# Kernel tuning notes

Measured on AMD Instinct MI355X. Metric: run time of the kernel, lower is better.

Reference implementation:

```python
import jax, jax.numpy as jnp
import numpy as np

FG_THRESH = 0.5
BG_THRESH_HI = 0.5
BG_THRESH_LO = 0.1

NUM_ROIS = 8192
NUM_CLASSES = 20


def setup_inputs() -> dict:
    key = jax.random.key(0)
    k1, k2, k3, k4 = jax.random.split(key, 4)
    S = jax.random.uniform(k1, (NUM_ROIS, NUM_CLASSES), dtype=jnp.float32)
    # symmetric IoU-like matrix in [0,1] with unit diagonal
    R = jax.random.uniform(k2, (NUM_ROIS, NUM_ROIS), dtype=jnp.float32)
    U = 0.5 * (R + R.T)
    U = U.at[jnp.arange(NUM_ROIS), jnp.arange(NUM_ROIS)].set(1.0)
    # image-level multi-hot labels (float 0/1), ensure at least plausible positives
    L = (jax.random.uniform(k3, (1, NUM_CLASSES), dtype=jnp.float32) > 0.5).astype(jnp.float32)
    L = L.at[0, 0].set(1.0)  # guarantee at least one present class
    CW = jax.random.uniform(k4, (1, NUM_CLASSES), dtype=jnp.float32)
    return {"S": S, "U": U, "L": L, "CW": CW}


def reference(S, U, L, CW):
    """OICR-style ROI labeling (top_k=1 seed per present class).

    For each image-level class c with L[c] > 0, the highest-scoring ROI is the
    seed. Every ROI is assigned to the seed class with which it has maximal
    IoU. ROIs with best IoU >= fg_threshold become foreground (label c+1),
    ROIs with best IoU in [bg_thresh_lo, bg_thresh_hi) become background
    (label 0); all others are ignored (label -1, weight 0). Weights come
    from the per-class weight CW of the matched seed class.
    Returns (RL [N] int32, RW [N] float32).
    """
    valid = L[0] > 0                                   # [C]
    # seed ROI per class: argmax score (top_k = 1)
    seed_idx = jnp.argmax(S, axis=0)                   # [C]
    # IoU of every ROI to each class seed; invalid classes masked out
    iou = U[:, seed_idx]                               # [N, C]
    iou = jnp.where(valid[None, :], iou, -1.0)
    best_c = jnp.argmax(iou, axis=1)                   # [N]
    best_iou = jnp.max(iou, axis=1)                    # [N]

    is_fg = best_iou >= FG_THRESH
    is_bg = (best_iou < BG_THRESH_HI) & (best_iou >= BG_THRESH_LO)

    RL = jnp.where(is_fg, best_c.astype(jnp.int32) + 1,
                   jnp.where(is_bg, 0, -1)).astype(jnp.int32)
    w = CW[0][best_c]                                  # [N]
    RW = jnp.where(is_fg | is_bg, w, 0.0).astype(jnp.float32)
    return (RL, RW)
```

## Files before the change

kernel.cpp:

```cpp
#include <hip/hip_runtime.h>

#define NUM_ROIS 8192
#define NUM_CLASSES 20
#define FG_THRESH 0.5f
#define BG_HI 0.5f
#define BG_LO 0.1f

__global__ void roilabel_seed_argmax(const float* __restrict__ S,
                                     int* __restrict__ seeds) {
    const int c = blockIdx.x;
    const int t = threadIdx.x;

    float best_v = -__builtin_inff();
    int best_i = NUM_ROIS;

    for (int r = t; r < NUM_ROIS; r += 256) {
        float v = S[r * NUM_CLASSES + c];
        if (v > best_v) { best_v = v; best_i = r; }
    }

    __shared__ float sv[256];
    __shared__ int   si[256];
    sv[t] = best_v;
    si[t] = best_i;
    __syncthreads();

    for (int off = 128; off > 0; off >>= 1) {
        if (t < off) {
            float v2 = sv[t + off];
            int   i2 = si[t + off];
            if (v2 > sv[t] || (v2 == sv[t] && i2 < si[t])) {
                sv[t] = v2;
                si[t] = i2;
            }
        }
        __syncthreads();
    }
    if (t == 0) seeds[c] = si[0];
}

__global__ void roilabel_assign(const float* __restrict__ U,
                                const float* __restrict__ L,
                                const float* __restrict__ CW,
                                const int* __restrict__ seeds,
                                float* __restrict__ out) {
    __shared__ int   s_seed[NUM_CLASSES];
    __shared__ int   s_valid[NUM_CLASSES];
    __shared__ float s_cw[NUM_CLASSES];

    const int t = threadIdx.x;
    if (t < NUM_CLASSES) {
        s_seed[t]  = seeds[t];
        s_valid[t] = (L[t] > 0.0f) ? 1 : 0;
        s_cw[t]    = CW[t];
    }
    __syncthreads();

    const int i = blockIdx.x * blockDim.x + t;
    if (i >= NUM_ROIS) return;

    const float* __restrict__ row = U + (size_t)i * NUM_ROIS;

    float best_iou = -2.0f;
    int best_c = 0;
    #pragma unroll
    for (int c = 0; c < NUM_CLASSES; ++c) {
        float v = s_valid[c] ? row[s_seed[c]] : -1.0f;
        if (v > best_iou) { best_iou = v; best_c = c; }
    }

    const bool is_fg = (best_iou >= FG_THRESH);
    const bool is_bg = (best_iou < BG_HI) && (best_iou >= BG_LO);

    int   rl = is_fg ? (best_c + 1) : (is_bg ? 0 : -1);
    float rw = (is_fg || is_bg) ? s_cw[best_c] : 0.0f;

    out[i]            = (float)rl;
    out[NUM_ROIS + i] = rw;
}

extern "C" void kernel_launch(void* const* d_in, const int* in_sizes, int n_in,
                              void* d_out, int out_size, void* d_ws, size_t ws_size,
                              hipStream_t stream) {
    const float* S  = (const float*)d_in[0];
    const float* U  = (const float*)d_in[1];
    const float* L  = (const float*)d_in[2];
    const float* CW = (const float*)d_in[3];
    float* out = (float*)d_out;
    int* seeds = (int*)d_ws;

    roilabel_seed_argmax<<<NUM_CLASSES, 256, 0, stream>>>(S, seeds);
    roilabel_assign<<<NUM_ROIS / 256, 256, 0, stream>>>(U, L, CW, seeds, out);
}
```

Before: 20.90 us.

## Fuse seed argmax into assign kernel with redundant per-block float4 scan

Merges the two kernels into one, removing the second launch and the workspace round-trip for the seed indices. Each of the 32 blocks redundantly scans all of S (8192x20) with float4 loads, tracking the argmax for all 20 classes per thread, then does a shared-memory tree reduction over 20 classes before doing the IoU assignment. The redundant scan multiplies S reads by 32 (served largely from L2) and raises register and LDS use (about 40KB of shared memory), which in exchange for one fewer launch may lower occupancy.

```diff
diff --git a/kernel.cpp b/kernel.cpp
--- a/kernel.cpp
+++ b/kernel.cpp
@@ -5,60 +5,66 @@
 #define FG_THRESH 0.5f
 #define BG_HI 0.5f
 #define BG_LO 0.1f
+#define NBLK (NUM_ROIS / 256)
 
-__global__ void roilabel_seed_argmax(const float* __restrict__ S,
-                                     int* __restrict__ seeds) {
-    const int c = blockIdx.x;
+__global__ __launch_bounds__(256) void roilabel_fused(
+    const float* __restrict__ S,
+    const float* __restrict__ U,
+    const float* __restrict__ L,
+    const float* __restrict__ CW,
+    float* __restrict__ out) {
+
     const int t = threadIdx.x;
 
-    float best_v = -__builtin_inff();
-    int best_i = NUM_ROIS;
+    float bv[NUM_CLASSES];
+    int   bi[NUM_CLASSES];
+    #pragma unroll
+    for (int c = 0; c < NUM_CLASSES; ++c) { bv[c] = -__builtin_inff(); bi[c] = 0; }
 
+    const float4* __restrict__ S4 = (const float4*)S;
     for (int r = t; r < NUM_ROIS; r += 256) {
-        float v = S[r * NUM_CLASSES + c];
-        if (v > best_v) { best_v = v; best_i = r; }
+        #pragma unroll
+        for (int j = 0; j < 5; ++j) {
+            float4 v = S4[r * 5 + j];
+            if (v.x > bv[j * 4 + 0]) { bv[j * 4 + 0] = v.x; bi[j * 4 + 0] = r; }
+            if (v.y > bv[j * 4 + 1]) { bv[j * 4 + 1] = v.y; bi[j * 4 + 1] = r; }
+            if (v.z > bv[j * 4 + 2]) { bv[j * 4 + 2] = v.z; bi[j * 4 + 2] = r; }
+            if (v.w > bv[j * 4 + 3]) { bv[j * 4 + 3] = v.w; bi[j * 4 + 3] = r; }
+        }
     }
 
-    __shared__ float sv[256];
-    __shared__ int   si[256];
-    sv[t] = best_v;
-    si[t] = best_i;
+    __shared__ float sv[NUM_CLASSES][256];
+    __shared__ int   si[NUM_CLASSES][256];
+    #pragma unroll
+    for (int c = 0; c < NUM_CLASSES; ++c) { sv[c][t] = bv[c]; si[c][t] = bi[c]; }
     __syncthreads();
 
     for (int off = 128; off > 0; off >>= 1) {
         if (t < off) {
-            float v2 = sv[t + off];
-            int   i2 = si[t + off];
-            if (v2 > sv[t] || (v2 == sv[t] && i2 < si[t])) {
-                sv[t] = v2;
-                si[t] = i2;
+            #pragma unroll
+            for (int c = 0; c < NUM_CLASSES; ++c) {
+                float v2 = sv[c][t + off];
+                int   i2 = si[c][t + off];
+                if (v2 > sv[c][t] || (v2 == sv[c][t] && i2 < si[c][t])) {
+                    sv[c][t] = v2;
+                    si[c][t] = i2;
+                }
             }
         }
         __syncthreads();
     }
-    if (t == 0) seeds[c] = si[0];
-}
 
-__global__ void roilabel_assign(const float* __restrict__ U,
-                                const float* __restrict__ L,
-                                const float* __restrict__ CW,
-                                const int* __restrict__ seeds,
-                                float* __restrict__ out) {
     __shared__ int   s_seed[NUM_CLASSES];
     __shared__ int   s_valid[NUM_CLASSES];
     __shared__ float s_cw[NUM_CLASSES];
-
-    const int t = threadIdx.x;
     if (t < NUM_CLASSES) {
-        s_seed[t]  = seeds[t];
+        s_seed[t]  = si[t][0];
         s_valid[t] = (L[t] > 0.0f) ? 1 : 0;
         s_cw[t]    = CW[t];
     }
     __syncthreads();
 
-    const int i = blockIdx.x * blockDim.x + t;
-    if (i >= NUM_ROIS) return;
-
+    const int i = blockIdx.x * 256 + t;
     const float* __restrict__ row = U + (size_t)i * NUM_ROIS;
 
     float best_iou = -2.0f;
@@ -87,8 +93,6 @@
     const float* L  = (const float*)d_in[2];
     const float* CW = (const float*)d_in[3];
     float* out = (float*)d_out;
-    int* seeds = (int*)d_ws;
 
-    roilabel_seed_argmax<<<NUM_CLASSES, 256, 0, stream>>>(S, seeds);
-    roilabel_assign<<<NUM_ROIS / 256, 256, 0, stream>>>(U, L, CW, seeds, out);
+    roilabel_fused<<<NBLK, 256, 0, stream>>>(S, U, L, CW, out);
 }
```

After: 36.19 us. 73.1% more time.
